# Kernel tuning notes

Measured on AMD Instinct MI355X. Metric: run time of the kernel, lower is better.

Reference implementation:

```python
import jax, jax.numpy as jnp
import numpy as np
import math

NUM_GROUPS = 32
EPS = 1e-5

def group_norm(x, weight, bias):
    # x: (b, c, h, w); normalize over (c/G, h, w) within each group
    b, c, h, w = x.shape
    xg = x.reshape(b, NUM_GROUPS, c // NUM_GROUPS, h, w)
    mean = xg.mean(axis=(2, 3, 4), keepdims=True)
    var = xg.var(axis=(2, 3, 4), keepdims=True)
    xg = (xg - mean) * jax.lax.rsqrt(var + EPS)
    xn = xg.reshape(b, c, h, w)
    return xn * weight[None, :, None, None] + bias[None, :, None, None]


def setup_inputs() -> dict:
    key = jax.random.key(0)
    ks = jax.random.split(key, 3)
    b, c, h, w = 8, 256, 64, 64
    x = jax.random.normal(ks[0], (b, c, h, w), dtype=jnp.float32)
    gn_weight = jnp.ones((c,), dtype=jnp.float32)
    gn_bias = jnp.zeros((c,), dtype=jnp.float32)
    qkv_w = jax.random.normal(ks[1], (3 * c, c), dtype=jnp.float32) * (1.0 / math.sqrt(c))
    qkv_b = jnp.zeros((3 * c,), dtype=jnp.float32)
    out_w = jax.random.normal(ks[2], (c, c), dtype=jnp.float32) * (1.0 / math.sqrt(c))
    out_b = jnp.zeros((c,), dtype=jnp.float32)
    return {"x": x, "gn_weight": gn_weight, "gn_bias": gn_bias,
            "qkv_w": qkv_w, "qkv_b": qkv_b, "out_w": out_w, "out_b": out_b}


def reference(x, gn_weight, gn_bias, qkv_w, qkv_b, out_w, out_b):
    b, c, h, w = x.shape
    xn = group_norm(x, gn_weight, gn_bias)
    # 1x1 conv == per-pixel matmul: (3c, c) x (b, c, h, w) -> (b, 3c, h, w)
    qkv = jnp.einsum('oc,bchw->bohw', qkv_w, xn) + qkv_b[None, :, None, None]
    q, k, v = jnp.split(qkv, 3, axis=1)
    hw = h * w
    q = q.transpose(0, 2, 3, 1).reshape(b, hw, c)   # (b, hw, c)
    k = k.reshape(b, c, hw)                          # (b, c, hw)
    v = v.transpose(0, 2, 3, 1).reshape(b, hw, c)   # (b, hw, c)
    scale = 1.0 / math.sqrt(c)
    attn = jax.nn.softmax(jnp.einsum('bic,bcj->bij', q, k) * scale, axis=-1)
    out = jnp.einsum('bij,bjc->bic', attn, v)        # (b, hw, c)
    out = out.reshape(b, h, w, c).transpose(0, 3, 1, 2)  # (b, c, h, w)
    out = jnp.einsum('oc,bchw->bohw', out_w, out) + out_b[None, :, None, None]
    return out + x
```

## Files before the change

### kernel.cpp

```cpp
#include <hip/hip_runtime.h>

#define HW 4096
#define NC 256
#define NB 8
#define GN_EPS 1e-5f

typedef short bf16x8 __attribute__((ext_vector_type(8)));
typedef float f32x4 __attribute__((ext_vector_type(4)));
typedef float f32x16 __attribute__((ext_vector_type(16)));

#define MFMA16 __builtin_amdgcn_mfma_f32_16x16x32_bf16
#define MFMA32 __builtin_amdgcn_mfma_f32_32x32x16_bf16

#define SWZ(row) ((((row) & 7) ^ (((row) >> 3) & 7)) << 4)

#define QSCALE 0.09016844f

__device__ __forceinline__ unsigned short f2bf(float f) {
  unsigned int u = __float_as_uint(f);
  u = (u + 0x7FFFu + ((u >> 16) & 1u)) >> 16;
  return (unsigned short)u;
}
__device__ __forceinline__ float bf2f(unsigned short h) {
  return __uint_as_float(((unsigned int)h) << 16);
}

__device__ __forceinline__ void gload16(const void* g, void* l) {
  __builtin_amdgcn_global_load_lds(
      (const __attribute__((address_space(1))) void*)g,
      (__attribute__((address_space(3))) void*)l, 16, 0, 0);
}

__global__ void gn_stats_kernel(const float* __restrict__ x,
                                const float* __restrict__ gnw,
                                const float* __restrict__ gnb,
                                float* __restrict__ s_arr,
                                float* __restrict__ t_arr) {
  int bg = blockIdx.x;
  int b = bg >> 5, g = bg & 31;
  const float4* base = (const float4*)(x + ((size_t)b * NC + g * 8) * HW);
  int tid = threadIdx.x;
  float s = 0.f, ss = 0.f;
  for (int it = 0; it < 32; ++it) {
    float4 v = base[tid + it * 256];
    s += v.x + v.y + v.z + v.w;
    ss += v.x * v.x + v.y * v.y + v.z * v.z + v.w * v.w;
  }
  for (int off = 32; off; off >>= 1) {
    s += __shfl_down(s, off);
    ss += __shfl_down(ss, off);
  }
  __shared__ float red[8];
  __shared__ float bc[2];
  int wave = tid >> 6, lane = tid & 63;
  if (lane == 0) { red[wave] = s; red[4 + wave] = ss; }
  __syncthreads();
  if (tid == 0) {
    float S = red[0] + red[1] + red[2] + red[3];
    float SS = red[4] + red[5] + red[6] + red[7];
    float mean = S * (1.f / 32768.f);
    float var = SS * (1.f / 32768.f) - mean * mean;
    bc[0] = mean;
    bc[1] = rsqrtf(var + GN_EPS);
  }
  __syncthreads();
  if (tid < 8) {
    int c = g * 8 + tid;
    float sv = bc[1] * gnw[c];
    s_arr[b * NC + c] = sv;
    t_arr[b * NC + c] = gnb[c] - bc[0] * sv;
  }
}

__global__ void wconv_kernel(const float* __restrict__ qkvw,
                             const float* __restrict__ ow,
                             unsigned short* __restrict__ wb) {
  int i = blockIdx.x * 256 + threadIdx.x;
  int off = i * 8;
  const float* src = (i < 24576) ? (qkvw + off) : (ow + (off - 196608));
  float4 a = *(const float4*)src;
  float4 c = *(const float4*)(src + 4);
  *(ushort4*)(wb + off) =
      make_ushort4(f2bf(a.x), f2bf(a.y), f2bf(a.z), f2bf(a.w));
  *(ushort4*)(wb + off + 4) =
      make_ushort4(f2bf(c.x), f2bf(c.y), f2bf(c.z), f2bf(c.w));
}

__global__ __launch_bounds__(256) void gn_apply_kernel(
    const float* __restrict__ x, const float* __restrict__ s_arr,
    const float* __restrict__ t_arr, unsigned short* __restrict__ xt) {
  int b = blockIdx.z;
  int p0 = blockIdx.x * 64, c0 = blockIdx.y * 64;
  int tid = threadIdx.x;
  __shared__ unsigned short tl[64 * 64];
  char* tB = (char*)tl;
  int cl = tid >> 4, p4 = tid & 15;
#pragma unroll
  for (int rep = 0; rep < 4; ++rep) {
    int c = cl + rep * 16;
    float4 xv = *(const float4*)(x + ((size_t)b * NC + c0 + c) * HW + p0 + p4 * 4);
    float sc = s_arr[b * NC + c0 + c];
    float tc = t_arr[b * NC + c0 + c];
    float vals[4] = {xv.x, xv.y, xv.z, xv.w};
#pragma unroll
    for (int i = 0; i < 4; ++i) {
      int p = p4 * 4 + i;
      *(unsigned short*)(tB + ((p * 128 + c * 2) ^ SWZ(p))) =
          f2bf(vals[i] * sc + tc);
    }
  }
  __syncthreads();
#pragma unroll
  for (int rep = 0; rep < 2; ++rep) {
    int p = (tid >> 3) + rep * 32;
    int c8 = (tid & 7) * 8;
    bf16x8 v = *(const bf16x8*)(tB + ((p * 128 + c8 * 2) ^ SWZ(p)));
    *(bf16x8*)(xt + ((size_t)b * HW + p0 + p) * NC + c0 + c8) = v;
  }
}

__global__ __launch_bounds__(256) void qkv_gemm_kernel(
    const unsigned short* __restrict__ xt, const unsigned short* __restrict__ wb,
    const float* __restrict__ bias, unsigned short* __restrict__ qb,
    unsigned short* __restrict__ kc_, unsigned short* __restrict__ vc) {
  int b = blockIdx.z;
  int p0 = blockIdx.x * 64;
  int o0 = blockIdx.y * 128;
  int tid = threadIdx.x;
  int wave = tid >> 6, lane = tid & 63;
  int l15 = lane & 15, q4 = lane >> 4;
  int wm = wave >> 1, wn = wave & 1;
  __shared__ unsigned short a_lds[2][64 * 64];
  __shared__ unsigned short b_lds[2][128 * 64];

  const char* xtb = (const char*)(xt + ((size_t)b * HW + p0) * NC);
  const char* wbb = (const char*)wb + o0 * 512;
  unsigned int asrc[2], bsrc[4];
#pragma unroll
  for (int i = 0; i < 2; ++i) {
    int dk = wave * 2048 + i * 1024 + lane * 16;
    int row = dk >> 7;
    asrc[i] = row * 512 + ((dk & 127) ^ SWZ(row));
  }
#pragma unroll
  for (int i = 0; i < 4; ++i) {
    int dk = wave * 4096 + i * 1024 + lane * 16;
    int row = dk >> 7;
    bsrc[i] = row * 512 + ((dk & 127) ^ SWZ(row));
  }

  f32x4 acc[2][4];
#pragma unroll
  for (int i = 0; i < 2; ++i)
#pragma unroll
    for (int j = 0; j < 4; ++j) acc[i][j] = (f32x4){0.f, 0.f, 0.f, 0.f};

#pragma unroll
  for (int i = 0; i < 2; ++i)
    gload16(xtb + asrc[i], (char*)a_lds[0] + wave * 2048 + i * 1024 + lane * 16);
#pragma unroll
  for (int i = 0; i < 4; ++i)
    gload16(wbb + bsrc[i], (char*)b_lds[0] + wave * 4096 + i * 1024 + lane * 16);
  __syncthreads();

  for (int kc = 0; kc < 4; ++kc) {
    int cur = kc & 1;
    if (kc < 3) {
      int koff = (kc + 1) * 128;
#pragma unroll
      for (int i = 0; i < 2; ++i)
        gload16(xtb + asrc[i] + koff,
                (char*)a_lds[cur ^ 1] + wave * 2048 + i * 1024 + lane * 16);
#pragma unroll
      for (int i = 0; i < 4; ++i)
        gload16(wbb + bsrc[i] + koff,
                (char*)b_lds[cur ^ 1] + wave * 4096 + i * 1024 + lane * 16);
    }
    const char* aB = (const char*)a_lds[cur];
    const char* bB = (const char*)b_lds[cur];
#pragma unroll
    for (int kk = 0; kk < 2; ++kk) {
      bf16x8 af[2], bfv[4];
#pragma unroll
      for (int pb = 0; pb < 2; ++pb) {
        int row = wm * 32 + pb * 16 + l15;
        af[pb] = *(const bf16x8*)(aB + ((row * 128 + kk * 64 + q4 * 16) ^ SWZ(row)));
      }
#pragma unroll
      for (int ob = 0; ob < 4; ++ob) {
        int row = wn * 64 + ob * 16 + l15;
        bfv[ob] = *(const bf16x8*)(bB + ((row * 128 + kk * 64 + q4 * 16) ^ SWZ(row)));
      }
#pragma unroll
      for (int pb = 0; pb < 2; ++pb)
#pragma unroll
        for (int ob = 0; ob < 4; ++ob)
          acc[pb][ob] = MFMA16(af[pb], bfv[ob], acc[pb][ob], 0, 0, 0);
    }
    __syncthreads();
  }

  for (int pb = 0; pb < 2; ++pb) {
    for (int ob = 0; ob < 4; ++ob) {
      int og = o0 + wn * 64 + ob * 16 + l15;
      int tsel = og >> 8, oc = og & 255;
      float bi = bias[og];
      if (tsel == 2) {
        int p = p0 + wm * 32 + pb * 16 + q4 * 4;
        ushort4 pk4 = make_ushort4(
            f2bf(acc[pb][ob][0] + bi), f2bf(acc[pb][ob][1] + bi),
            f2bf(acc[pb][ob][2] + bi), f2bf(acc[pb][ob][3] + bi));
        *(ushort4*)(vc + (((size_t)b * 512 + (p >> 3)) * 256 + oc) * 8 + (p & 7)) =
            pk4;
      } else {
        for (int r = 0; r < 4; ++r) {
          int p = p0 + wm * 32 + pb * 16 + q4 * 4 + r;
          float val = acc[pb][ob][r] + bi;
          if (tsel == 0) {
            qb[((size_t)b * HW + p) * NC + oc] = f2bf(val * QSCALE);
          } else {
            kc_[((size_t)(b * 32 + (oc >> 3)) * HW + p) * 8 + (oc & 7)] = f2bf(val);
          }
        }
      }
    }
  }
}

__global__ __launch_bounds__(256, 2) void flash_attn_kernel(
    const unsigned short* __restrict__ qb, const unsigned short* __restrict__ kc_,
    const unsigned short* __restrict__ vc, unsigned short* __restrict__ Oh0,
    unsigned short* __restrict__ Oh1, float* __restrict__ Lb) {
  int b = blockIdx.x & 7;
  int qt = (blockIdx.x >> 3) & 31;
  int half = blockIdx.x >> 8;
  int tid = threadIdx.x;
  int wave = tid >> 6, lane = tid & 63;
  int l31 = lane & 31;
  int hi = lane >> 5;

  __shared__ unsigned short k_lds[2][8192];
  __shared__ unsigned short v_lds[2][8192];

  int j0b = half * 2048;

  const char* kp[4];
  const char* vp[4];
  {
    const char* kcb = (const char*)(kc_ + (size_t)b * 32 * HW * 8);
    const char* vcb = (const char*)(vc + (size_t)b * 512 * NC * 8);
#pragma unroll
    for (int i = 0; i < 4; ++i) {
      kp[i] = kcb + (size_t)((tid >> 5) + i * 8) * 65536 +
              (size_t)(j0b + (tid & 31)) * 16;
      vp[i] = vcb + (size_t)((j0b >> 3) + i) * 4096 + tid * 16;
    }
  }

  bf16x8 qf[16];
  {
    const unsigned short* qrow =
        qb + ((size_t)b * HW + qt * 128 + wave * 32 + l31) * NC;
#pragma unroll
    for (int kb = 0; kb < 16; ++kb)
      qf[kb] = *(const bf16x8*)(qrow + kb * 16 + hi * 8);
  }

  f32x16 acc[8];
#pragma unroll
  for (int nb = 0; nb < 8; ++nb)
#pragma unroll
    for (int i = 0; i < 16; ++i) acc[nb][i] = 0.f;
  float m_r = -1e30f, l_r = 0.f;

#pragma unroll
  for (int i = 0; i < 4; ++i)
    gload16(kp[i], (char*)k_lds[0] + tid * 16 + i * 4096);
#pragma unroll
  for (int i = 0; i < 4; ++i)
    gload16(vp[i], (char*)v_lds[0] + tid * 16 + i * 4096);
  __syncthreads();

  for (int t = 0; t < 64; ++t) {
    int cur = t & 1;
    if (t < 63) {
#pragma unroll
      for (int i = 0; i < 4; ++i) {
        kp[i] += 512;
        gload16(kp[i], (char*)k_lds[cur ^ 1] + tid * 16 + i * 4096);
      }
#pragma unroll
      for (int i = 0; i < 4; ++i) {
        vp[i] += 16384;
        gload16(vp[i], (char*)v_lds[cur ^ 1] + tid * 16 + i * 4096);
      }
    }
    const char* kB = (const char*)k_lds[cur];
    const char* vB = (const char*)v_lds[cur];

    f32x16 p;
#pragma unroll
    for (int i = 0; i < 16; ++i) p[i] = 0.f;
    __builtin_amdgcn_s_setprio(1);
#pragma unroll
    for (int kb = 0; kb < 16; ++kb) {
      bf16x8 kf = *(const bf16x8*)(kB + (kb * 2 + hi) * 512 + l31 * 16);
      p = MFMA32(kf, qf[kb], p, 0, 0, 0);
    }
    __builtin_amdgcn_s_setprio(0);

    float pmax;
    {
      float t0 = fmaxf(p[0], p[1]), t1 = fmaxf(p[2], p[3]);
      float t2 = fmaxf(p[4], p[5]), t3 = fmaxf(p[6], p[7]);
      float t4 = fmaxf(p[8], p[9]), t5 = fmaxf(p[10], p[11]);
      float t6 = fmaxf(p[12], p[13]), t7 = fmaxf(p[14], p[15]);
      float u0 = fmaxf(t0, t1), u1 = fmaxf(t2, t3);
      float u2 = fmaxf(t4, t5), u3 = fmaxf(t6, t7);
      pmax = fmaxf(fmaxf(u0, u1), fmaxf(u2, u3));
    }
    pmax = fmaxf(pmax, __shfl_xor(pmax, 32));
    if (!__all(pmax - m_r <= 12.0f)) {
      float mn = fmaxf(m_r, pmax);
      float sf = exp2f(m_r - mn);
      m_r = mn;
      l_r *= sf;
#pragma unroll
      for (int reg = 0; reg < 16; ++reg) {
        float sfr = __shfl(sf, (reg & 3) + 8 * (reg >> 2) + 4 * hi);
#pragma unroll
        for (int nb = 0; nb < 8; ++nb) acc[nb][reg] *= sfr;
      }
    }
#pragma unroll
    for (int i = 0; i < 16; ++i) p[i] = __builtin_amdgcn_exp2f(p[i] - m_r);
    float rs;
    {
      float t0 = p[0] + p[1], t1 = p[2] + p[3];
      float t2 = p[4] + p[5], t3 = p[6] + p[7];
      float t4 = p[8] + p[9], t5 = p[10] + p[11];
      float t6 = p[12] + p[13], t7 = p[14] + p[15];
      float u0 = t0 + t1, u1 = t2 + t3, u2 = t4 + t5, u3 = t6 + t7;
      rs = (u0 + u1) + (u2 + u3);
    }
    rs += __shfl_xor(rs, 32);
    l_r += rs;

    int pk[8];
#pragma unroll
    for (int i = 0; i < 8; ++i) {
      int r;
      asm("v_cvt_pk_bf16_f32 %0, %1, %2"
          : "=v"(r)
          : "v"(p[2 * i]), "v"(p[2 * i + 1]));
      pk[i] = r;
    }
    union PU { int w[4]; bf16x8 v; } pu[2];
#pragma unroll
    for (int kb = 0; kb < 2; ++kb) {
      int base = 4 * kb;
      int pushA = hi ? pk[base + 0] : pk[base + 2];
      int pushB = hi ? pk[base + 1] : pk[base + 3];
      int shA = __shfl_xor(pushA, 32);
      int shB = __shfl_xor(pushB, 32);
      pu[kb].w[0] = hi ? shA : pk[base + 0];
      pu[kb].w[1] = hi ? shB : pk[base + 1];
      pu[kb].w[2] = hi ? pk[base + 2] : shA;
      pu[kb].w[3] = hi ? pk[base + 3] : shB;
    }

    __builtin_amdgcn_s_setprio(1);
#pragma unroll
    for (int nb = 0; nb < 8; ++nb) {
#pragma unroll
      for (int kb = 0; kb < 2; ++kb) {
        bf16x8 vf = *(const bf16x8*)(vB + (kb * 2 + hi) * 4096 +
                                     (nb * 32 + l31) * 16);
        acc[nb] = MFMA32(pu[kb].v, vf, acc[nb], 0, 0, 0);
      }
    }
    __builtin_amdgcn_s_setprio(0);
    __syncthreads();
  }

  float linv = 1.f / l_r;
  unsigned short* Ohp = (half ? Oh1 : Oh0) +
                        ((size_t)b * HW + qt * 128 + wave * 32) * NC;
#pragma unroll
  for (int reg = 0; reg < 16; ++reg) {
    int row = (reg & 3) + 8 * (reg >> 2) + 4 * hi;
    float lr = __shfl(linv, row);
#pragma unroll
    for (int nb = 0; nb < 8; ++nb)
      Ohp[(size_t)row * NC + nb * 32 + l31] = f2bf(acc[nb][reg] * lr);
  }
  if (lane < 32) {
    float* Lp = Lb + (size_t)half * NB * HW;
    Lp[(size_t)b * HW + qt * 128 + wave * 32 + lane] = m_r + log2f(l_r);
  }
}

__global__ __launch_bounds__(256) void outproj_kernel(
    const unsigned short* __restrict__ owb, const float* __restrict__ obias,
    const unsigned short* __restrict__ Oh0, const unsigned short* __restrict__ Oh1,
    const float* __restrict__ Lb, const float* __restrict__ x,
    float* __restrict__ out) {
  int b = blockIdx.y;
  int p0 = blockIdx.x * 64;
  int tid = threadIdx.x;
  int wave = tid >> 6, lane = tid & 63;
  int l15 = lane & 15, q4 = lane >> 4;
  __shared__ unsigned short aw_lds[256 * 64];
  __shared__ unsigned short bt_lds[64 * 64];
  char* aB = (char*)aw_lds;
  char* bB = (char*)bt_lds;

  unsigned int wsrc[8];
#pragma unroll
  for (int i = 0; i < 8; ++i) {
    int dk = wave * 8192 + i * 1024 + lane * 16;
    int row = dk >> 7;
    wsrc[i] = row * 512 + ((dk & 127) ^ SWZ(row));
  }
  const char* owbb = (const char*)owb;

  f32x4 acc[4][4];
  for (int i = 0; i < 4; ++i)
    for (int j = 0; j < 4; ++j) acc[i][j] = (f32x4){0.f, 0.f, 0.f, 0.f};

  for (int kc0 = 0; kc0 < 256; kc0 += 64) {
    __syncthreads();
#pragma unroll
    for (int i = 0; i < 8; ++i)
      gload16(owbb + wsrc[i] + kc0 * 2,
              aB + wave * 8192 + i * 1024 + lane * 16);
    for (int it = 0; it < 2; ++it) {
      int idx = tid + it * 256;
      int p = idx >> 3, c8i = idx & 7;
      int row = p0 + p;
      float L1 = Lb[(size_t)b * HW + row];
      float L2 = Lb[(size_t)(NB + b) * HW + row];
      float w1 = 1.f / (1.f + exp2f(L2 - L1));
      float w2 = 1.f - w1;
      const unsigned short* o1p = Oh0 + ((size_t)b * HW + row) * NC + kc0 + c8i * 8;
      const unsigned short* o2p = Oh1 + ((size_t)b * HW + row) * NC + kc0 + c8i * 8;
      uint4 ra = *(const uint4*)o1p;
      uint4 rb = *(const uint4*)o2p;
      unsigned int aw[4] = {ra.x, ra.y, ra.z, ra.w};
      unsigned int bw[4] = {rb.x, rb.y, rb.z, rb.w};
      unsigned int outw[4];
      for (int i = 0; i < 4; ++i) {
        float lo = w1 * bf2f((unsigned short)(aw[i] & 0xffffu)) +
                   w2 * bf2f((unsigned short)(bw[i] & 0xffffu));
        float hic = w1 * bf2f((unsigned short)(aw[i] >> 16)) +
                    w2 * bf2f((unsigned short)(bw[i] >> 16));
        int r;
        asm("v_cvt_pk_bf16_f32 %0, %1, %2" : "=v"(r) : "v"(lo), "v"(hic));
        outw[i] = (unsigned int)r;
      }
      *(uint4*)(bB + ((p * 128 + c8i * 16) ^ SWZ(p))) =
          make_uint4(outw[0], outw[1], outw[2], outw[3]);
    }
    __syncthreads();
#pragma unroll
    for (int kk = 0; kk < 2; ++kk) {
      bf16x8 af[4], bfv[4];
      for (int obk = 0; obk < 4; ++obk) {
        int row = wave * 64 + obk * 16 + l15;
        af[obk] = *(const bf16x8*)(aB + ((row * 128 + kk * 64 + q4 * 16) ^ SWZ(row)));
      }
      for (int pb = 0; pb < 4; ++pb) {
        int row = pb * 16 + l15;
        bfv[pb] = *(const bf16x8*)(bB + ((row * 128 + kk * 64 + q4 * 16) ^ SWZ(row)));
      }
      for (int obk = 0; obk < 4; ++obk)
        for (int pb = 0; pb < 4; ++pb)
          acc[obk][pb] = MFMA16(af[obk], bfv[pb], acc[obk][pb], 0, 0, 0);
    }
  }
  for (int obk = 0; obk < 4; ++obk)
    for (int pb = 0; pb < 4; ++pb)
      for (int r = 0; r < 4; ++r) {
        int o = wave * 64 + obk * 16 + q4 * 4 + r;
        int p = p0 + pb * 16 + l15;
        size_t gi = ((size_t)b * NC + o) * HW + p;
        out[gi] = acc[obk][pb][r] + obias[o] + x[gi];
      }
}

extern "C" void kernel_launch(void* const* d_in, const int* in_sizes, int n_in,
                              void* d_out, int out_size, void* d_ws, size_t ws_size,
                              hipStream_t stream) {
  (void)in_sizes; (void)n_in; (void)out_size; (void)ws_size;
  const float* x = (const float*)d_in[0];
  const float* gnw = (const float*)d_in[1];
  const float* gnb = (const float*)d_in[2];
  const float* qkvw = (const float*)d_in[3];
  const float* qkvb = (const float*)d_in[4];
  const float* ow = (const float*)d_in[5];
  const float* obias = (const float*)d_in[6];
  float* out = (float*)d_out;

  char* ws = (char*)d_ws;
  float* s_arr = (float*)ws;
  float* t_arr = s_arr + NB * NC;
  size_t tsz = (size_t)NB * HW * NC;
  unsigned short* qb = (unsigned short*)(ws + 16384);
  unsigned short* kc_ = qb + tsz;
  unsigned short* Oh0 = kc_ + tsz;
  unsigned short* vc = Oh0 + tsz;
  unsigned short* Oh1 = vc + tsz;
  unsigned short* xt = Oh1;
  float* Lb = (float*)(Oh1 + tsz);
  unsigned short* wb = (unsigned short*)(Lb + 2 * NB * HW);
  unsigned short* owb = wb + 196608;

  hipLaunchKernelGGL(gn_stats_kernel, dim3(NB * 32), dim3(256), 0, stream,
                     x, gnw, gnb, s_arr, t_arr);
  hipLaunchKernelGGL(wconv_kernel, dim3(128), dim3(256), 0, stream,
                     qkvw, ow, wb);
  hipLaunchKernelGGL(gn_apply_kernel, dim3(64, 4, NB), dim3(256), 0, stream,
                     x, s_arr, t_arr, xt);
  hipLaunchKernelGGL(qkv_gemm_kernel, dim3(64, 6, NB), dim3(256), 0, stream,
                     xt, wb, qkvb, qb, kc_, vc);
  hipLaunchKernelGGL(flash_attn_kernel, dim3(512), dim3(256), 0, stream,
                     qb, kc_, vc, Oh0, Oh1, Lb);
  hipLaunchKernelGGL(outproj_kernel, dim3(64, NB), dim3(256), 0, stream,
                     owb, obias, Oh0, Oh1, Lb, x, out);
}
```

Before: 208.0 us.

## Split attention keys three ways and single-buffer V for higher occupancy

Flash attention now splits the key range into three chunks instead of two, launching 768 blocks, and outproj merges three partial outputs using log-sum-exp weights. V is reduced to a single LDS buffer with an extra barrier per iteration, so LDS fits three blocks per CU, and launch bounds are raised to 3. The aim is more resident waves per CU to hide latency. The risks are register pressure or spilling under the tighter VGPR budget, an exposed V load, and an extra partial-output buffer to write and read. It falls back to a two-way split when the workspace is too small.

```diff
diff --git a/kernel.cpp b/kernel.cpp
--- a/kernel.cpp
+++ b/kernel.cpp
@@ -227,22 +227,26 @@
   }
 }
 
-__global__ __launch_bounds__(256, 2) void flash_attn_kernel(
+__global__ __launch_bounds__(256, 3) void flash_attn_kernel(
     const unsigned short* __restrict__ qb, const unsigned short* __restrict__ kc_,
     const unsigned short* __restrict__ vc, unsigned short* __restrict__ Oh0,
-    unsigned short* __restrict__ Oh1, float* __restrict__ Lb) {
+    unsigned short* __restrict__ Oh1, unsigned short* __restrict__ Oh2,
+    float* __restrict__ Lb, int4 starts) {
   int b = blockIdx.x & 7;
   int qt = (blockIdx.x >> 3) & 31;
-  int half = blockIdx.x >> 8;
+  int js = blockIdx.x >> 8;
   int tid = threadIdx.x;
   int wave = tid >> 6, lane = tid & 63;
   int l31 = lane & 31;
   int hi = lane >> 5;
 
+  int s0 = (js == 0) ? starts.x : (js == 1 ? starts.y : starts.z);
+  int s1 = (js == 0) ? starts.y : (js == 1 ? starts.z : starts.w);
+  int nt = s1 - s0;
+  int j0b = s0 * 32;
+
   __shared__ unsigned short k_lds[2][8192];
-  __shared__ unsigned short v_lds[2][8192];
-
-  int j0b = half * 2048;
+  __shared__ unsigned short v_lds[8192];
 
   const char* kp[4];
   const char* vp[4];
@@ -278,25 +282,27 @@
     gload16(kp[i], (char*)k_lds[0] + tid * 16 + i * 4096);
 #pragma unroll
   for (int i = 0; i < 4; ++i)
-    gload16(vp[i], (char*)v_lds[0] + tid * 16 + i * 4096);
-  __syncthreads();
-
-  for (int t = 0; t < 64; ++t) {
+    gload16(vp[i], (char*)v_lds + tid * 16 + i * 4096);
+
+  for (int t = 0; t < nt; ++t) {
     int cur = t & 1;
-    if (t < 63) {
+    __syncthreads();
+    if (t < nt - 1) {
 #pragma unroll
       for (int i = 0; i < 4; ++i) {
         kp[i] += 512;
         gload16(kp[i], (char*)k_lds[cur ^ 1] + tid * 16 + i * 4096);
       }
+    }
+    if (t >= 1) {
 #pragma unroll
       for (int i = 0; i < 4; ++i) {
         vp[i] += 16384;
-        gload16(vp[i], (char*)v_lds[cur ^ 1] + tid * 16 + i * 4096);
+        gload16(vp[i], (char*)v_lds + tid * 16 + i * 4096);
       }
     }
     const char* kB = (const char*)k_lds[cur];
-    const char* vB = (const char*)v_lds[cur];
+    const char* vB = (const char*)v_lds;
 
     f32x16 p;
 #pragma unroll
@@ -369,6 +375,8 @@
       pu[kb].w[3] = hi ? pk[base + 3] : shB;
     }
 
+    __syncthreads();
+
     __builtin_amdgcn_s_setprio(1);
 #pragma unroll
     for (int nb = 0; nb < 8; ++nb) {
@@ -380,11 +388,10 @@
       }
     }
     __builtin_amdgcn_s_setprio(0);
-    __syncthreads();
   }
 
   float linv = 1.f / l_r;
-  unsigned short* Ohp = (half ? Oh1 : Oh0) +
+  unsigned short* Ohp = (js == 0 ? Oh0 : (js == 1 ? Oh1 : Oh2)) +
                         ((size_t)b * HW + qt * 128 + wave * 32) * NC;
 #pragma unroll
   for (int reg = 0; reg < 16; ++reg) {
@@ -395,7 +402,7 @@
       Ohp[(size_t)row * NC + nb * 32 + l31] = f2bf(acc[nb][reg] * lr);
   }
   if (lane < 32) {
-    float* Lp = Lb + (size_t)half * NB * HW;
+    float* Lp = Lb + (size_t)js * NB * HW;
     Lp[(size_t)b * HW + qt * 128 + wave * 32 + lane] = m_r + log2f(l_r);
   }
 }
@@ -403,8 +410,8 @@
 __global__ __launch_bounds__(256) void outproj_kernel(
     const unsigned short* __restrict__ owb, const float* __restrict__ obias,
     const unsigned short* __restrict__ Oh0, const unsigned short* __restrict__ Oh1,
-    const float* __restrict__ Lb, const float* __restrict__ x,
-    float* __restrict__ out) {
+    const unsigned short* __restrict__ Oh2, const float* __restrict__ Lb,
+    const float* __restrict__ x, float* __restrict__ out, int ns) {
   int b = blockIdx.y;
   int p0 = blockIdx.x * 64;
   int tid = threadIdx.x;
@@ -438,22 +445,30 @@
       int idx = tid + it * 256;
       int p = idx >> 3, c8i = idx & 7;
       int row = p0 + p;
-      float L1 = Lb[(size_t)b * HW + row];
-      float L2 = Lb[(size_t)(NB + b) * HW + row];
-      float w1 = 1.f / (1.f + exp2f(L2 - L1));
-      float w2 = 1.f - w1;
-      const unsigned short* o1p = Oh0 + ((size_t)b * HW + row) * NC + kc0 + c8i * 8;
-      const unsigned short* o2p = Oh1 + ((size_t)b * HW + row) * NC + kc0 + c8i * 8;
-      uint4 ra = *(const uint4*)o1p;
-      uint4 rb = *(const uint4*)o2p;
+      float L0 = Lb[(size_t)b * HW + row];
+      float L1 = Lb[(size_t)(NB + b) * HW + row];
+      float L2 = (ns == 3) ? Lb[(size_t)(2 * NB + b) * HW + row] : -1e30f;
+      float M = fmaxf(fmaxf(L0, L1), L2);
+      float e0 = exp2f(L0 - M), e1 = exp2f(L1 - M);
+      float e2 = (ns == 3) ? exp2f(L2 - M) : 0.f;
+      float inv = 1.f / (e0 + e1 + e2);
+      float w0 = e0 * inv, w1 = e1 * inv, w2 = e2 * inv;
+      size_t ro = ((size_t)b * HW + row) * NC + kc0 + c8i * 8;
+      uint4 ra = *(const uint4*)(Oh0 + ro);
+      uint4 rb = *(const uint4*)(Oh1 + ro);
+      uint4 rc = (ns == 3) ? *(const uint4*)(Oh2 + ro)
+                           : make_uint4(0, 0, 0, 0);
       unsigned int aw[4] = {ra.x, ra.y, ra.z, ra.w};
       unsigned int bw[4] = {rb.x, rb.y, rb.z, rb.w};
+      unsigned int cw[4] = {rc.x, rc.y, rc.z, rc.w};
       unsigned int outw[4];
       for (int i = 0; i < 4; ++i) {
-        float lo = w1 * bf2f((unsigned short)(aw[i] & 0xffffu)) +
-                   w2 * bf2f((unsigned short)(bw[i] & 0xffffu));
-        float hic = w1 * bf2f((unsigned short)(aw[i] >> 16)) +
-                    w2 * bf2f((unsigned short)(bw[i] >> 16));
+        float lo = w0 * bf2f((unsigned short)(aw[i] & 0xffffu)) +
+                   w1 * bf2f((unsigned short)(bw[i] & 0xffffu)) +
+                   w2 * bf2f((unsigned short)(cw[i] & 0xffffu));
+        float hic = w0 * bf2f((unsigned short)(aw[i] >> 16)) +
+                    w1 * bf2f((unsigned short)(bw[i] >> 16)) +
+                    w2 * bf2f((unsigned short)(cw[i] >> 16));
         int r;
         asm("v_cvt_pk_bf16_f32 %0, %1, %2" : "=v"(r) : "v"(lo), "v"(hic));
         outw[i] = (unsigned int)r;
@@ -491,7 +506,7 @@
 extern "C" void kernel_launch(void* const* d_in, const int* in_sizes, int n_in,
                               void* d_out, int out_size, void* d_ws, size_t ws_size,
                               hipStream_t stream) {
-  (void)in_sizes; (void)n_in; (void)out_size; (void)ws_size;
+  (void)in_sizes; (void)n_in; (void)out_size;
   const float* x = (const float*)d_in[0];
   const float* gnw = (const float*)d_in[1];
   const float* gnb = (const float*)d_in[2];
@@ -505,15 +520,24 @@
   float* s_arr = (float*)ws;
   float* t_arr = s_arr + NB * NC;
   size_t tsz = (size_t)NB * HW * NC;
+
+  size_t need3 = 16384 + 6 * tsz * 2 + 3 * NB * HW * 4 + 262144 * 2;
+  int ns = (ws_size >= need3) ? 3 : 2;
+
   unsigned short* qb = (unsigned short*)(ws + 16384);
   unsigned short* kc_ = qb + tsz;
   unsigned short* Oh0 = kc_ + tsz;
   unsigned short* vc = Oh0 + tsz;
   unsigned short* Oh1 = vc + tsz;
-  unsigned short* xt = Oh1;
-  float* Lb = (float*)(Oh1 + tsz);
-  unsigned short* wb = (unsigned short*)(Lb + 2 * NB * HW);
+  unsigned short* Oh2 = (ns == 3) ? (Oh1 + tsz) : Oh1;
+  float* Lb = (float*)(Oh2 + tsz);
+  unsigned short* wb = (unsigned short*)(Lb + 3 * NB * HW);
   unsigned short* owb = wb + 196608;
+  unsigned short* xt = (ns == 3) ? Oh2 : Oh1;
+  if (ns == 2) Lb = (float*)(Oh1 + tsz);
+  if (ns == 2) { wb = (unsigned short*)(Lb + 3 * NB * HW); owb = wb + 196608; }
+
+  int4 starts = (ns == 3) ? make_int4(0, 43, 86, 128) : make_int4(0, 64, 128, 128);
 
   hipLaunchKernelGGL(gn_stats_kernel, dim3(NB * 32), dim3(256), 0, stream,
                      x, gnw, gnb, s_arr, t_arr);
@@ -523,8 +547,8 @@
                      x, s_arr, t_arr, xt);
   hipLaunchKernelGGL(qkv_gemm_kernel, dim3(64, 6, NB), dim3(256), 0, stream,
                      xt, wb, qkvb, qb, kc_, vc);
-  hipLaunchKernelGGL(flash_attn_kernel, dim3(512), dim3(256), 0, stream,
-                     qb, kc_, vc, Oh0, Oh1, Lb);
+  hipLaunchKernelGGL(flash_attn_kernel, dim3(256 * ns), dim3(256), 0, stream,
+                     qb, kc_, vc, Oh0, Oh1, Oh2, Lb, starts);
   hipLaunchKernelGGL(outproj_kernel, dim3(64, NB), dim3(256), 0, stream,
-                     owb, obias, Oh0, Oh1, Lb, x, out);
-}
+                     owb, obias, Oh0, Oh1, Oh2, Lb, x, out, ns);
+}
```

After: 460.1 us. 121% more time.
